# Optimization experiments

Measured on AMD Instinct MI355X. Metric: run time of the kernel, lower is better.

## Reference

```python
import jax, jax.numpy as jnp
import numpy as np

# Mega (Flash-Quad) encoder layer: MultiHeadEMA + moving-average gated chunked attention + ScaleNorm
L, B, D = 2048, 16, 512        # seq_len, batch, embed_dim (fairseq L,B,D layout)
H, Z, NDIM = 1024, 128, 2      # hdim, zdim, EMA ndim
CHUNK = 128                    # Flash-Quad chunk size
MAXPOS = 1024                  # SimpleRelativePositionalBias max positions
EPS = 1e-6                     # ScaleNorm eps


def setup_inputs() -> dict:
    key = jax.random.key(0)
    ks = jax.random.split(key, 16)
    def nrm(k, shape, s=0.02):
        return jax.random.normal(k, shape, jnp.float32) * s
    return dict(
        x=jax.random.normal(ks[0], (L, B, D), jnp.float32),
        # MultiHeadEMA params (bidirectional -> kernel_dim = 2*D)
        ema_delta=nrm(ks[1], (2 * D, NDIM, 1), 1.0),
        ema_alpha=nrm(ks[2], (2 * D, NDIM, 1), 1.0),
        ema_beta=nrm(ks[3], (2 * D, NDIM, 1), 0.02),
        ema_gamma=nrm(ks[4], (2 * D, NDIM), 1.0),
        ema_omega=nrm(ks[5], (D,), 1.0),
        # projections
        Wv=nrm(ks[6], (D, H)), bv=jnp.zeros((H,), jnp.float32),
        Wmx=nrm(ks[7], (D, Z + H + 2 * D)), bmx=jnp.zeros((Z + H + 2 * D,), jnp.float32),
        Wh=nrm(ks[8], (H, D)), bh=jnp.zeros((D,), jnp.float32),
        # per-dim q/k affine (gamma/beta) on shared z
        qk_gamma=nrm(ks[9], (2, Z), 0.1) + 1.0,
        qk_beta=nrm(ks[10], (2, Z), 0.1),
        # simple relative positional bias over chunk length
        rel_pos_bias=nrm(ks[11], (2 * MAXPOS - 1,), 0.02),
        # ScaleNorm scalar
        norm_scalar=jnp.ones((), jnp.float32),
    )


def _ema(x, delta, alpha, beta, gamma, omega):
    """Bidirectional multi-dim damped EMA via FFT convolution. x: (L,B,D) -> (L,B,D)."""
    Lx, Bx, Dx = x.shape
    residual = x * omega
    xt = jnp.transpose(x, (1, 2, 0))                      # B,D,L
    p = jax.nn.sigmoid(delta)                             # 2D,n,1
    q = 1.0 - p * jax.nn.sigmoid(alpha)                   # 2D,n,1 in (0,1)
    vander = jnp.arange(Lx, dtype=jnp.float32)[None, None, :] * jnp.log(q)  # 2D,n,L
    kern = jnp.einsum('dnl,dn->dl', (p * beta) * jnp.exp(vander),
                      gamma * (1.0 / np.sqrt(NDIM)))      # 2D,L
    k1, k2 = kern[:Dx], kern[Dx:]
    # combined causal + anticausal kernel of length 2L-1, input left-padded by L-1
    kc = jnp.pad(k1, ((0, 0), (Lx - 1, 0))) + jnp.pad(k2[:, ::-1], ((0, 0), (0, Lx - 1)))
    xp = jnp.pad(xt, ((0, 0), (0, 0), (Lx - 1, 0)))
    n = 2 * (2 * Lx - 1)
    out = jnp.fft.irfft(jnp.fft.rfft(xp, n=n) * jnp.fft.rfft(kc, n=n), n=n)
    out = out[..., 2 * Lx - 2: 2 * Lx - 2 + Lx]           # B,D,L
    return jax.nn.silu(jnp.transpose(out, (2, 0, 1)) + residual)


def _forward(x, ema_delta, ema_alpha, ema_beta, ema_gamma, ema_omega,
             Wv, bv, Wmx, bmx, Wh, bh, qk_gamma, qk_beta, rel_pos_bias, norm_scalar):
    Lx, Bx, Dx = x.shape
    residual = x
    v = jax.nn.silu(x @ Wv + bv)                          # L,B,H
    mx = _ema(x, ema_delta, ema_alpha, ema_beta, ema_gamma, ema_omega)  # L,B,D
    base = mx @ Wmx + bmx                                 # L,B,D+Z+H+D
    u = jax.nn.sigmoid(base[..., :Dx])                    # update gate
    zr = jax.nn.silu(base[..., Dx:Dx + Z + H])
    hx = base[..., Dx + Z + H:]
    z, r = zr[..., :Z], zr[..., Z:]                       # shared z, reset gate r
    zqk = z[..., None, :] * qk_gamma + qk_beta            # L,B,2,Z
    nc = Lx // CHUNK
    q = jnp.transpose(zqk[..., 0, :], (1, 0, 2)).reshape(Bx, nc, CHUNK, Z)
    k = jnp.transpose(zqk[..., 1, :], (1, 0, 2)).reshape(Bx, nc, CHUNK, Z)
    vc = jnp.transpose(v, (1, 0, 2)).reshape(Bx, nc, CHUNK, H)
    # Toeplitz relative bias: bias[i,j] = rel_pos_bias[MAXPOS-1 + j - i]
    idx = (MAXPOS - 1) + jnp.arange(CHUNK)[None, :] - jnp.arange(CHUNK)[:, None]
    bias = rel_pos_bias[idx]                              # C,C
    qk = jnp.einsum('bnqz,bnkz->bnqk', q * (Z ** -0.5), k) + bias
    attn = jax.nn.softmax(qk, axis=-1)                    # B,nc,C,C
    h = jnp.einsum('bnqk,bnkh->bnqh', attn, vc).reshape(Bx, Lx, H)
    h = jnp.transpose(h, (1, 0, 2))                       # L,B,H
    h = jax.nn.silu(hx + (h * r) @ Wh + bh)               # L,B,D
    out = residual + u * (h - residual)                   # addcmul gated residual
    ms = jnp.mean(out * out, axis=-1, keepdims=True)      # ScaleNorm
    out = norm_scalar * out * jax.lax.rsqrt(ms + EPS)
    return out, attn


def reference(x, ema_delta, ema_alpha, ema_beta, ema_gamma, ema_omega,
              Wv, bv, Wmx, bmx, Wh, bh, qk_gamma, qk_beta, rel_pos_bias, norm_scalar):
    return _forward(x, ema_delta, ema_alpha, ema_beta, ema_gamma, ema_omega,
                    Wv, bv, Wmx, bmx, Wh, bh, qk_gamma, qk_beta, rel_pos_bias, norm_scalar)
```

## Files before the change

### kernel.cpp

```cpp
#include <hip/hip_runtime.h>
#include <math.h>

#define L_DIM 2048
#define B_DIM 16
#define D_DIM 512
#define H_DIM 1024
#define Z_DIM 128
#define NC    16
#define BASE_N 2176
#define ROWS  (L_DIM*B_DIM)
#define NSEG  32
#define SLEN  64
#define CHAINS 8192

typedef unsigned short bf16_t;
typedef __attribute__((ext_vector_type(8))) short short8;
typedef __attribute__((ext_vector_type(4))) float f32x4;

__device__ __forceinline__ float sigmoidf_(float x){ return 1.f/(1.f+__expf(-x)); }
__device__ __forceinline__ float siluf_(float x){ return x/(1.f+__expf(-x)); }
__device__ __forceinline__ float fbits(unsigned int b){ union{unsigned int i; float f;} c; c.i=b; return c.f; }
__device__ __forceinline__ unsigned short f2bf(float f){
  union{float f; unsigned int i;} c; c.f=f;
  unsigned int r = c.i + 0x7FFFu + ((c.i>>16)&1u);
  return (unsigned short)(r>>16);
}
__device__ __forceinline__ float bf2f(unsigned short u){ return fbits(((unsigned int)u)<<16); }

__device__ __forceinline__ void load8(const float* __restrict__ p, float* d){
  float4 a = *(const float4*)p; float4 b = *(const float4*)(p+4);
  d[0]=a.x; d[1]=a.y; d[2]=a.z; d[3]=a.w; d[4]=b.x; d[5]=b.y; d[6]=b.z; d[7]=b.w;
}
__device__ __forceinline__ void load8(const bf16_t* __restrict__ p, float* d){
  uint4 u = *(const uint4*)p;
  d[0]=fbits(u.x<<16); d[1]=fbits(u.x&0xFFFF0000u);
  d[2]=fbits(u.y<<16); d[3]=fbits(u.y&0xFFFF0000u);
  d[4]=fbits(u.z<<16); d[5]=fbits(u.z&0xFFFF0000u);
  d[6]=fbits(u.w<<16); d[7]=fbits(u.w&0xFFFF0000u);
}
__device__ __forceinline__ void store8bf(bf16_t* p, const float* v){
  uint4 s;
  s.x = (unsigned int)f2bf(v[0]) | ((unsigned int)f2bf(v[1])<<16);
  s.y = (unsigned int)f2bf(v[2]) | ((unsigned int)f2bf(v[3])<<16);
  s.z = (unsigned int)f2bf(v[4]) | ((unsigned int)f2bf(v[5])<<16);
  s.w = (unsigned int)f2bf(v[6]) | ((unsigned int)f2bf(v[7])<<16);
  *(uint4*)p = s;
}

__device__ __forceinline__ void glds16(const void* g, void* l) {
  __builtin_amdgcn_global_load_lds(
      (const __attribute__((address_space(1))) unsigned int*)g,
      (__attribute__((address_space(3))) unsigned int*)l, 16, 0, 0);
}

__global__ __launch_bounds__(256) void transpose_cvt_kernel(
    const float* __restrict__ W, bf16_t* __restrict__ Wt, int K, int N)
{
  __shared__ float t[32][33];
  int bx = blockIdx.x, by = blockIdx.y;
  int lx = threadIdx.x & 31, ly = threadIdx.x >> 5;
  #pragma unroll
  for (int i = 0; i < 32; i += 8)
    t[ly+i][lx] = W[(size_t)(by*32+ly+i)*N + bx*32 + lx];
  __syncthreads();
  #pragma unroll
  for (int i = 0; i < 32; i += 8)
    Wt[(size_t)(bx*32+ly+i)*K + by*32 + lx] = f2bf(t[lx][ly+i]);
}

__global__ __launch_bounds__(256) void ema_carry_kernel(
    const float* __restrict__ x, const float* __restrict__ delta,
    const float* __restrict__ alpha, bf16_t* __restrict__ xb,
    float* __restrict__ carry)
{
  int idx = blockIdx.x*256 + threadIdx.x;
  int d = idx & 511, c = idx & 8191, s = idx >> 13;
  float qf0 = 1.f - sigmoidf_(delta[d*2+0])*sigmoidf_(alpha[d*2+0]);
  float qf1 = 1.f - sigmoidf_(delta[d*2+1])*sigmoidf_(alpha[d*2+1]);
  int dd = d + 512;
  float qb0 = 1.f - sigmoidf_(delta[dd*2+0])*sigmoidf_(alpha[dd*2+0]);
  float qb1 = 1.f - sigmoidf_(delta[dd*2+1])*sigmoidf_(alpha[dd*2+1]);
  size_t off = (size_t)s*SLEN*CHAINS + c;
  float h0=0.f, h1=0.f;
  #pragma unroll
  for (int t = 0; t < SLEN; ++t) {
    size_t a = off + (size_t)t*CHAINS;
    float xv = x[a];
    xb[a] = f2bf(xv);
    h0 = fmaf(qf0, h0, xv); h1 = fmaf(qf1, h1, xv);
  }
  float g0=0.f, g1=0.f;
  #pragma unroll
  for (int t = SLEN-1; t >= 0; --t) {
    float xv = bf2f(xb[off + (size_t)t*CHAINS]);
    g0 = fmaf(qb0, g0, xv); g1 = fmaf(qb1, g1, xv);
  }
  carry[(size_t)s*CHAINS + c]              = h0;
  carry[(size_t)s*CHAINS + c + 262144]     = h1;
  carry[(size_t)s*CHAINS + c + 524288]     = g0;
  carry[(size_t)s*CHAINS + c + 786432]     = g1;
}

__global__ __launch_bounds__(256) void ema_combine_kernel(
    const float* __restrict__ delta, const float* __restrict__ alpha,
    float* __restrict__ carry)
{
  int c = blockIdx.x*256 + threadIdx.x;
  int d = c & 511;
  float qf0 = 1.f - sigmoidf_(delta[d*2+0])*sigmoidf_(alpha[d*2+0]);
  float qf1 = 1.f - sigmoidf_(delta[d*2+1])*sigmoidf_(alpha[d*2+1]);
  int dd = d + 512;
  float qb0 = 1.f - sigmoidf_(delta[dd*2+0])*sigmoidf_(alpha[dd*2+0]);
  float qb1 = 1.f - sigmoidf_(delta[dd*2+1])*sigmoidf_(alpha[dd*2+1]);
  float df0=qf0, df1=qf1, db0=qb0, db1=qb1;
  #pragma unroll
  for (int i = 0; i < 6; ++i) { df0*=df0; df1*=df1; db0*=db0; db1*=db1; }
  float h0=0.f, h1=0.f;
  for (int s = 0; s < NSEG; ++s) {
    size_t a = (size_t)s*CHAINS + c;
    float t0 = carry[a], t1 = carry[a+262144];
    carry[a] = h0; carry[a+262144] = h1;
    h0 = fmaf(df0, h0, t0); h1 = fmaf(df1, h1, t1);
  }
  float g0=0.f, g1=0.f;
  for (int s = NSEG-1; s >= 0; --s) {
    size_t a = (size_t)s*CHAINS + c;
    float t0 = carry[a+524288], t1 = carry[a+786432];
    carry[a+524288] = g0; carry[a+786432] = g1;
    g0 = fmaf(db0, g0, t0); g1 = fmaf(db1, g1, t1);
  }
}

__global__ __launch_bounds__(256) void ema_apply_kernel(
    const bf16_t* __restrict__ xb, const float* __restrict__ delta,
    const float* __restrict__ alpha, const float* __restrict__ beta,
    const float* __restrict__ gamma, const float* __restrict__ omega,
    const float* __restrict__ carry, bf16_t* __restrict__ mx)
{
  int idx = blockIdx.x*256 + threadIdx.x;
  int d = idx & 511, c = idx & 8191, s = idx >> 13;
  const float rs = 0.70710678118654752f;
  float pf0 = sigmoidf_(delta[d*2+0]), pf1 = sigmoidf_(delta[d*2+1]);
  float qf0 = 1.f - pf0*sigmoidf_(alpha[d*2+0]);
  float qf1 = 1.f - pf1*sigmoidf_(alpha[d*2+1]);
  float cf0 = pf0*beta[d*2+0]*gamma[d*2+0]*rs;
  float cf1 = pf1*beta[d*2+1]*gamma[d*2+1]*rs;
  int dd = d + 512;
  float pb0 = sigmoidf_(delta[dd*2+0]), pb1 = sigmoidf_(delta[dd*2+1]);
  float qb0 = 1.f - pb0*sigmoidf_(alpha[dd*2+0]);
  float qb1 = 1.f - pb1*sigmoidf_(alpha[dd*2+1]);
  float cb0 = pb0*beta[dd*2+0]*gamma[dd*2+0]*rs;
  float cb1 = pb1*beta[dd*2+1]*gamma[dd*2+1]*rs;
  float om = omega[d];
  size_t off = (size_t)s*SLEN*CHAINS + c;
  float h0 = carry[(size_t)s*CHAINS + c];
  float h1 = carry[(size_t)s*CHAINS + c + 262144];
  float yv[SLEN];
  #pragma unroll
  for (int t = 0; t < SLEN; ++t) {
    float xv = bf2f(xb[off + (size_t)t*CHAINS]);
    h0 = fmaf(qf0, h0, xv); h1 = fmaf(qf1, h1, xv);
    yv[t] = fmaf(cf0, h0, cf1*h1);
  }
  float g0 = carry[(size_t)s*CHAINS + c + 524288];
  float g1 = carry[(size_t)s*CHAINS + c + 786432];
  #pragma unroll
  for (int t = SLEN-1; t >= 0; --t) {
    size_t a = off + (size_t)t*CHAINS;
    float xv = bf2f(xb[a]);
    g0 = fmaf(qb0, g0, xv); g1 = fmaf(qb1, g1, xv);
    float sv = yv[t] + fmaf(cb0, g0, cb1*g1) + xv*om;
    mx[a] = f2bf(siluf_(sv));
  }
}

__global__ __launch_bounds__(256) void mfma_gemm_kernel(
    const bf16_t* __restrict__ A, const bf16_t* __restrict__ Bt,
    const float* __restrict__ bias, const bf16_t* __restrict__ Add, int addLd,
    bf16_t* __restrict__ C, int N, int K, int nT, int act)
{
  __shared__ __align__(16) char smem[34816];
  bf16_t* As = (bf16_t*)smem;
  bf16_t* Bs = (bf16_t*)(smem + 8192);
  bf16_t* Cs = (bf16_t*)smem;
  int flat = blockIdx.x;
  int xcd = flat & 7, g = flat >> 3;
  int mT8 = (int)(gridDim.x / (unsigned)nT) >> 3;
  int mt = xcd*mT8 + g / nT;
  int nt = g % nT;
  int m0 = mt*128, n0 = nt*128;
  int tid = threadIdx.x;
  int wave = tid >> 6, lane = tid & 63;
  int srow = lane >> 2, schunk = lane & 3;
  const bf16_t* Ag0 = A + (size_t)(m0 + wave*16 + srow)*K + schunk*8;
  const bf16_t* Ag1 = Ag0 + (size_t)64*K;
  const bf16_t* Bg0 = Bt + (size_t)(n0 + wave*16 + srow)*K + schunk*8;
  const bf16_t* Bg1 = Bg0 + (size_t)64*K;
  bf16_t* Asl0 = As + (wave*16)*32;
  bf16_t* Asl1 = As + (64 + wave*16)*32;
  bf16_t* Bsl0 = Bs + (wave*16)*32;
  bf16_t* Bsl1 = Bs + (64 + wave*16)*32;

  int wm = wave >> 1, wn = wave & 1;
  int fr = lane & 15, fq = lane >> 4;
  f32x4 acc[4][4];
  #pragma unroll
  for (int i = 0; i < 4; ++i)
    #pragma unroll
    for (int j = 0; j < 4; ++j)
      acc[i][j] = (f32x4){0.f,0.f,0.f,0.f};

  for (int k0 = 0; k0 < K; k0 += 32) {
    __syncthreads();
    glds16(Ag0 + k0, Asl0);
    glds16(Ag1 + k0, Asl1);
    glds16(Bg0 + k0, Bsl0);
    glds16(Bg1 + k0, Bsl1);
    __syncthreads();
    short8 af[4], bfr[4];
    #pragma unroll
    for (int mi = 0; mi < 4; ++mi)
      af[mi] = *(const short8*)&As[(wm*64 + mi*16 + fr)*32 + fq*8];
    #pragma unroll
    for (int ni = 0; ni < 4; ++ni)
      bfr[ni] = *(const short8*)&Bs[(wn*64 + ni*16 + fr)*32 + fq*8];
    #pragma unroll
    for (int mi = 0; mi < 4; ++mi)
      #pragma unroll
      for (int ni = 0; ni < 4; ++ni)
        acc[mi][ni] = __builtin_amdgcn_mfma_f32_16x16x32_bf16(
            af[mi], bfr[ni], acc[mi][ni], 0, 0, 0);
  }

  __syncthreads();
  #pragma unroll
  for (int ni = 0; ni < 4; ++ni) {
    int cl = wn*64 + ni*16 + fr;
    int gn = n0 + cl;
    float bv = bias[gn];
    #pragma unroll
    for (int mi = 0; mi < 4; ++mi) {
      #pragma unroll
      for (int r = 0; r < 4; ++r) {
        int ml = wm*64 + mi*16 + fq*4 + r;
        float val = acc[mi][ni][r] + bv;
        if (Add) val += bf2f(Add[(size_t)(m0+ml)*addLd + gn]);
        if (act == 1) val = siluf_(val);
        Cs[ml*136 + cl] = f2bf(val);
      }
    }
  }
  __syncthreads();
  int row = tid >> 1, c0 = (tid & 1)*64;
  #pragma unroll
  for (int q = 0; q < 8; ++q)
    *(uint4*)(C + (size_t)(m0+row)*N + n0 + c0 + q*8) =
        *(const uint4*)&Cs[row*136 + c0 + q*8];
}

__global__ __launch_bounds__(256) void mfma_gemm_v_kernel(
    const bf16_t* __restrict__ A, const bf16_t* __restrict__ Bt,
    const float* __restrict__ bias, bf16_t* __restrict__ vt, int nT, int K)
{
  __shared__ __align__(16) char smem[34816];
  bf16_t* As = (bf16_t*)smem;
  bf16_t* Bs = (bf16_t*)(smem + 8192);
  bf16_t* Cs = (bf16_t*)smem;
  const int N = H_DIM;
  int flat = blockIdx.x;
  int xcd = flat & 7, g = flat >> 3;
  int mT8 = (int)(gridDim.x / (unsigned)nT) >> 3;
  int mt = xcd*mT8 + g / nT;
  int nt = g % nT;
  int m0 = mt*128, n0 = nt*128;
  int tid = threadIdx.x;
  int wave = tid >> 6, lane = tid & 63;
  int srow = lane >> 2, schunk = lane & 3;
  const bf16_t* Ag0 = A + (size_t)(m0 + wave*16 + srow)*K + schunk*8;
  const bf16_t* Ag1 = Ag0 + (size_t)64*K;
  const bf16_t* Bg0 = Bt + (size_t)(n0 + wave*16 + srow)*K + schunk*8;
  const bf16_t* Bg1 = Bg0 + (size_t)64*K;
  bf16_t* Asl0 = As + (wave*16)*32;
  bf16_t* Asl1 = As + (64 + wave*16)*32;
  bf16_t* Bsl0 = Bs + (wave*16)*32;
  bf16_t* Bsl1 = Bs + (64 + wave*16)*32;

  int wm = wave >> 1, wn = wave & 1;
  int fr = lane & 15, fq = lane >> 4;
  f32x4 acc[4][4];
  #pragma unroll
  for (int i = 0; i < 4; ++i)
    #pragma unroll
    for (int j = 0; j < 4; ++j)
      acc[i][j] = (f32x4){0.f,0.f,0.f,0.f};

  for (int k0 = 0; k0 < K; k0 += 32) {
    __syncthreads();
    glds16(Ag0 + k0, Asl0);
    glds16(Ag1 + k0, Asl1);
    glds16(Bg0 + k0, Bsl0);
    glds16(Bg1 + k0, Bsl1);
    __syncthreads();
    short8 af[4], bfr[4];
    #pragma unroll
    for (int mi = 0; mi < 4; ++mi)
      af[mi] = *(const short8*)&As[(wm*64 + mi*16 + fr)*32 + fq*8];
    #pragma unroll
    for (int ni = 0; ni < 4; ++ni)
      bfr[ni] = *(const short8*)&Bs[(wn*64 + ni*16 + fr)*32 + fq*8];
    #pragma unroll
    for (int mi = 0; mi < 4; ++mi)
      #pragma unroll
      for (int ni = 0; ni < 4; ++ni)
        acc[mi][ni] = __builtin_amdgcn_mfma_f32_16x16x32_bf16(
            af[mi], bfr[ni], acc[mi][ni], 0, 0, 0);
  }

  __syncthreads();
  #pragma unroll
  for (int ni = 0; ni < 4; ++ni) {
    int cl = wn*64 + ni*16 + fr;
    float bv = bias[n0 + cl];
    #pragma unroll
    for (int mi = 0; mi < 4; ++mi) {
      #pragma unroll
      for (int r = 0; r < 4; ++r) {
        int ml = wm*64 + mi*16 + fq*4 + r;
        Cs[ml*136 + cl] = f2bf(siluf_(acc[mi][ni][r] + bv));
      }
    }
  }
  __syncthreads();
  int b = tid >> 4, h0l = (tid & 15)*8;
  int nchunk = mt >> 4, kbase = (mt & 15)*8;
  #pragma unroll
  for (int j = 0; j < 8; ++j) {
    int hl = h0l + j;
    uint4 s;
    unsigned int w0 = (unsigned int)Cs[(0*16 + b)*136 + hl] |
                      ((unsigned int)Cs[(1*16 + b)*136 + hl] << 16);
    unsigned int w1 = (unsigned int)Cs[(2*16 + b)*136 + hl] |
                      ((unsigned int)Cs[(3*16 + b)*136 + hl] << 16);
    unsigned int w2 = (unsigned int)Cs[(4*16 + b)*136 + hl] |
                      ((unsigned int)Cs[(5*16 + b)*136 + hl] << 16);
    unsigned int w3 = (unsigned int)Cs[(6*16 + b)*136 + hl] |
                      ((unsigned int)Cs[(7*16 + b)*136 + hl] << 16);
    s.x=w0; s.y=w1; s.z=w2; s.w=w3;
    *(uint4*)&vt[((size_t)(b*NC + nchunk)*H_DIM + n0 + hl)*128 + kbase] = s;
  }
}

__global__ __launch_bounds__(256) void attn_scores_mfma_kernel(
    const bf16_t* __restrict__ base, const float* __restrict__ qkg,
    const float* __restrict__ qkb, const float* __restrict__ rpb,
    float* __restrict__ attn_out, bf16_t* __restrict__ p_bf)
{
  __shared__ bf16_t qs[128*136];
  __shared__ bf16_t ks[128*136];
  int blk = blockIdx.x;
  int b = blk >> 4, n = blk & 15;
  int tid = threadIdx.x;
  {
    int r = tid >> 1, z0 = (tid & 1)*64;
    size_t rowoff = ((size_t)((n*128 + r)*B_DIM + b))*BASE_N + 512 + z0;
    #pragma unroll
    for (int cchunk = 0; cchunk < 8; ++cchunk) {
      float t8[8], qv[8], kv[8];
      load8(base + rowoff + cchunk*8, t8);
      #pragma unroll
      for (int j = 0; j < 8; ++j) {
        int z = z0 + cchunk*8 + j;
        float zs = siluf_(t8[j]);
        qv[j] = fmaf(zs, qkg[z],     qkb[z]);
        kv[j] = fmaf(zs, qkg[128+z], qkb[128+z]);
      }
      store8bf(&qs[r*136 + z0 + cchunk*8], qv);
      store8bf(&ks[r*136 + z0 + cchunk*8], kv);
    }
  }
  __syncthreads();
  int wave = tid >> 6, lane = tid & 63;
  int fr = lane & 15, fq = lane >> 4;
  f32x4 acc[2][8];
  #pragma unroll
  for (int i = 0; i < 2; ++i)
    #pragma unroll
    for (int j = 0; j < 8; ++j)
      acc[i][j] = (f32x4){0.f,0.f,0.f,0.f};
  #pragma unroll
  for (int kk = 0; kk < 4; ++kk) {
    short8 af[2], bfr[8];
    #pragma unroll
    for (int mi = 0; mi < 2; ++mi)
      af[mi] = *(const short8*)&qs[(wave*32 + mi*16 + fr)*136 + kk*32 + fq*8];
    #pragma unroll
    for (int ni = 0; ni < 8; ++ni)
      bfr[ni] = *(const short8*)&ks[(ni*16 + fr)*136 + kk*32 + fq*8];
    #pragma unroll
    for (int mi = 0; mi < 2; ++mi)
      #pragma unroll
      for (int ni = 0; ni < 8; ++ni)
        acc[mi][ni] = __builtin_amdgcn_mfma_f32_16x16x32_bf16(
            af[mi], bfr[ni], acc[mi][ni], 0, 0, 0);
  }
  const float scale = 0.08838834764831845f;
  float mrow[2][4], srow[2][4];
  #pragma unroll
  for (int mi = 0; mi < 2; ++mi)
    #pragma unroll
    for (int r = 0; r < 4; ++r) mrow[mi][r] = -1e30f;
  #pragma unroll
  for (int mi = 0; mi < 2; ++mi)
    #pragma unroll
    for (int ni = 0; ni < 8; ++ni)
      #pragma unroll
      for (int r = 0; r < 4; ++r) {
        int i = wave*32 + mi*16 + fq*4 + r;
        int j = ni*16 + fr;
        float v = fmaf(acc[mi][ni][r], scale, rpb[1023 + j - i]);
        acc[mi][ni][r] = v;
        mrow[mi][r] = fmaxf(mrow[mi][r], v);
      }
  #pragma unroll
  for (int mi = 0; mi < 2; ++mi)
    #pragma unroll
    for (int r = 0; r < 4; ++r) {
      float m = mrow[mi][r];
      m = fmaxf(m, __shfl_xor(m, 1));
      m = fmaxf(m, __shfl_xor(m, 2));
      m = fmaxf(m, __shfl_xor(m, 4));
      m = fmaxf(m, __shfl_xor(m, 8));
      mrow[mi][r] = m;
      srow[mi][r] = 0.f;
    }
  #pragma unroll
  for (int mi = 0; mi < 2; ++mi)
    #pragma unroll
    for (int ni = 0; ni < 8; ++ni)
      #pragma unroll
      for (int r = 0; r < 4; ++r) {
        float e = __expf(acc[mi][ni][r] - mrow[mi][r]);
        acc[mi][ni][r] = e;
        srow[mi][r] += e;
      }
  #pragma unroll
  for (int mi = 0; mi < 2; ++mi)
    #pragma unroll
    for (int r = 0; r < 4; ++r) {
      float s = srow[mi][r];
      s += __shfl_xor(s, 1);
      s += __shfl_xor(s, 2);
      s += __shfl_xor(s, 4);
      s += __shfl_xor(s, 8);
      srow[mi][r] = 1.f/s;
    }
  #pragma unroll
  for (int mi = 0; mi < 2; ++mi)
    #pragma unroll
    for (int r = 0; r < 4; ++r) {
      int i = wave*32 + mi*16 + fq*4 + r;
      size_t o = ((size_t)blk*128 + i)*128;
      #pragma unroll
      for (int ni = 0; ni < 8; ++ni) {
        float val = acc[mi][ni][r]*srow[mi][r];
        attn_out[o + ni*16 + fr] = val;
        p_bf[o + ni*16 + fr] = f2bf(val);
      }
    }
}

__global__ __launch_bounds__(256) void attn_pv_kernel(
    const bf16_t* __restrict__ p_bf, const bf16_t* __restrict__ vt,
    const bf16_t* __restrict__ base, bf16_t* __restrict__ hr)
{
  __shared__ __align__(16) char smem[34816];
  bf16_t* As = (bf16_t*)smem;
  bf16_t* Bs = (bf16_t*)(smem + 8192);
  bf16_t* Cs = (bf16_t*)smem;
  int blk = blockIdx.x >> 3, ht = blockIdx.x & 7;
  int b = blk >> 4, n = blk & 15;
  const int K = 128;
  int tid = threadIdx.x;
  int wave = tid >> 6, lane = tid & 63;
  int srow = lane >> 2, schunk = lane & 3;
  const bf16_t* A = p_bf + (size_t)blk*(128*128);
  const bf16_t* Bt = vt + ((size_t)blk*H_DIM + ht*128)*128;
  const bf16_t* Ag0 = A + (size_t)(wave*16 + srow)*K + schunk*8;
  const bf16_t* Ag1 = Ag0 + (size_t)64*K;
  const bf16_t* Bg0 = Bt + (size_t)(wave*16 + srow)*K + schunk*8;
  const bf16_t* Bg1 = Bg0 + (size_t)64*K;
  bf16_t* Asl0 = As + (wave*16)*32;
  bf16_t* Asl1 = As + (64 + wave*16)*32;
  bf16_t* Bsl0 = Bs + (wave*16)*32;
  bf16_t* Bsl1 = Bs + (64 + wave*16)*32;

  int wm = wave >> 1, wn = wave & 1;
  int fr = lane & 15, fq = lane >> 4;
  f32x4 acc[4][4];
  #pragma unroll
  for (int i = 0; i < 4; ++i)
    #pragma unroll
    for (int j = 0; j < 4; ++j)
      acc[i][j] = (f32x4){0.f,0.f,0.f,0.f};

  for (int k0 = 0; k0 < K; k0 += 32) {
    __syncthreads();
    glds16(Ag0 + k0, Asl0);
    glds16(Ag1 + k0, Asl1);
    glds16(Bg0 + k0, Bsl0);
    glds16(Bg1 + k0, Bsl1);
    __syncthreads();
    short8 af[4], bfr[4];
    #pragma unroll
    for (int mi = 0; mi < 4; ++mi)
      af[mi] = *(const short8*)&As[(wm*64 + mi*16 + fr)*32 + fq*8];
    #pragma unroll
    for (int ni = 0; ni < 4; ++ni)
      bfr[ni] = *(const short8*)&Bs[(wn*64 + ni*16 + fr)*32 + fq*8];
    #pragma unroll
    for (int mi = 0; mi < 4; ++mi)
      #pragma unroll
      for (int ni = 0; ni < 4; ++ni)
        acc[mi][ni] = __builtin_amdgcn_mfma_f32_16x16x32_bf16(
            af[mi], bfr[ni], acc[mi][ni], 0, 0, 0);
  }

  __syncthreads();
  #pragma unroll
  for (int ni = 0; ni < 4; ++ni) {
    int cl = wn*64 + ni*16 + fr;
    int hg = ht*128 + cl;
    #pragma unroll
    for (int mi = 0; mi < 4; ++mi) {
      #pragma unroll
      for (int r = 0; r < 4; ++r) {
        int ml = wm*64 + mi*16 + fq*4 + r;
        size_t rowg = (size_t)((n*128 + ml)*B_DIM + b);
        float rg = bf2f(base[rowg*BASE_N + 640 + hg]);
        Cs[ml*136 + cl] = f2bf(acc[mi][ni][r]*siluf_(rg));
      }
    }
  }
  __syncthreads();
  int row = tid >> 1, c0 = (tid & 1)*64;
  size_t rowg = (size_t)((n*128 + row)*B_DIM + b);
  #pragma unroll
  for (int q = 0; q < 8; ++q)
    *(uint4*)(hr + rowg*H_DIM + ht*128 + c0 + q*8) =
        *(const uint4*)&Cs[row*136 + c0 + q*8];
}

__global__ __launch_bounds__(64) void final_kernel(
    const float* __restrict__ x, const bf16_t* __restrict__ h2,
    const bf16_t* __restrict__ base, const float* __restrict__ ns,
    float* __restrict__ out)
{
  int row = blockIdx.x;
  int t = threadIdx.x;
  size_t ro = (size_t)row*D_DIM + t*8;
  float xv[8]; load8(x + ro, xv);
  float hv[8]; load8(h2 + ro, hv);
  float uv[8]; load8(base + (size_t)row*BASE_N + t*8, uv);
  float o[8];
  float ss = 0.f;
  #pragma unroll
  for (int i = 0; i < 8; ++i) {
    float u = sigmoidf_(uv[i]);
    o[i] = xv[i] + u*(hv[i] - xv[i]);
    ss += o[i]*o[i];
  }
  #pragma unroll
  for (int m = 1; m < 64; m <<= 1) ss += __shfl_xor(ss, m);
  float inv = rsqrtf(ss*(1.f/(float)D_DIM) + 1e-6f) * ns[0];
  float4 r0, r1;
  r0.x = o[0]*inv; r0.y = o[1]*inv; r0.z = o[2]*inv; r0.w = o[3]*inv;
  r1.x = o[4]*inv; r1.y = o[5]*inv; r1.z = o[6]*inv; r1.w = o[7]*inv;
  *(float4*)(out + ro) = r0;
  *(float4*)(out + ro + 4) = r1;
}

extern "C" void kernel_launch(void* const* d_in, const int* in_sizes, int n_in,
                              void* d_out, int out_size, void* d_ws, size_t ws_size,
                              hipStream_t stream)
{
  const float* x     = (const float*)d_in[0];
  const float* delta = (const float*)d_in[1];
  const float* alpha = (const float*)d_in[2];
  const float* beta  = (const float*)d_in[3];
  const float* gamma = (const float*)d_in[4];
  const float* omega = (const float*)d_in[5];
  const float* Wv    = (const float*)d_in[6];
  const float* bv    = (const float*)d_in[7];
  const float* Wmx   = (const float*)d_in[8];
  const float* bmx   = (const float*)d_in[9];
  const float* Wh    = (const float*)d_in[10];
  const float* bh    = (const float*)d_in[11];
  const float* qkg   = (const float*)d_in[12];
  const float* qkb   = (const float*)d_in[13];
  const float* rpb   = (const float*)d_in[14];
  const float* ns    = (const float*)d_in[15];

  float* out  = (float*)d_out;
  float* attn = out + (size_t)ROWS*D_DIM;

  char* outb = (char*)d_out;
  bf16_t* x_bf  = (bf16_t*)outb;
  bf16_t* p_bf  = (bf16_t*)outb;
  bf16_t* Wv_t  = (bf16_t*)(outb + 33554432ull);
  bf16_t* Wmx_t = (bf16_t*)(outb + 34603008ull);
  bf16_t* Wh_t  = (bf16_t*)(outb + 36831232ull);

  const size_t WS_NEED = 310378496ull;
  if (ws_size < WS_NEED) return;
  char* wsb = (char*)d_ws;
  bf16_t* mx_bf   = (bf16_t*)(wsb);
  bf16_t* vt      = (bf16_t*)(wsb + 33554432ull);
  bf16_t* base_bf = (bf16_t*)(wsb + 100663296ull);
  bf16_t* hr_bf   = (bf16_t*)(wsb + 243269632ull);
  float*  carry   = (float*)(wsb + 100663296ull);
  bf16_t* h2_bf   = mx_bf;

  transpose_cvt_kernel<<<dim3(32, 16), 256, 0, stream>>>(Wv,  Wv_t,  512, 1024);
  transpose_cvt_kernel<<<dim3(68, 16), 256, 0, stream>>>(Wmx, Wmx_t, 512, 2176);
  transpose_cvt_kernel<<<dim3(16, 32), 256, 0, stream>>>(Wh,  Wh_t,  1024, 512);
  ema_carry_kernel<<<1024, 256, 0, stream>>>(x, delta, alpha, x_bf, carry);
  ema_combine_kernel<<<32, 256, 0, stream>>>(delta, alpha, carry);
  ema_apply_kernel<<<1024, 256, 0, stream>>>(x_bf, delta, alpha, beta, gamma,
                                             omega, carry, mx_bf);
  mfma_gemm_v_kernel<<<2048, 256, 0, stream>>>(x_bf, Wv_t, bv, vt, 8, D_DIM);
  mfma_gemm_kernel<<<4352, 256, 0, stream>>>(
      mx_bf, Wmx_t, bmx, nullptr, 0, base_bf, BASE_N, D_DIM, 17, 0);
  attn_scores_mfma_kernel<<<B_DIM*NC, 256, 0, stream>>>(
      base_bf, qkg, qkb, rpb, attn, p_bf);
  attn_pv_kernel<<<2048, 256, 0, stream>>>(p_bf, vt, base_bf, hr_bf);
  mfma_gemm_kernel<<<1024, 256, 0, stream>>>(
      hr_bf, Wh_t, bh, base_bf + 1664, BASE_N, h2_bf, D_DIM, H_DIM, 4, 1);
  final_kernel<<<ROWS, 64, 0, stream>>>(x, h2_bf, base_bf, ns, out);
}
```

Baseline: 678.5 us.

## Double GEMM K-step to 64 with XOR-swizzled LDS and merge weight transposes

The shared MFMA GEMM main loop now stages 64-wide K slices per iteration instead of 32, which halves the number of barrier pairs per tile. The LDS layout is rotated per row so fragment reads avoid bank conflicts. The three weight transpose/convert launches are merged into one launch to cut launch overhead. The cost is a larger LDS footprint for the staged tiles, and the loop still has no double buffering.

```diff
diff --git a/kernel.cpp b/kernel.cpp
--- a/kernel.cpp
+++ b/kernel.cpp
@@ -53,11 +53,17 @@
       (__attribute__((address_space(3))) unsigned int*)l, 16, 0, 0);
 }
 
-__global__ __launch_bounds__(256) void transpose_cvt_kernel(
-    const float* __restrict__ W, bf16_t* __restrict__ Wt, int K, int N)
+__global__ __launch_bounds__(256) void transpose_all_kernel(
+    const float* __restrict__ Wv, const float* __restrict__ Wmx,
+    const float* __restrict__ Wh, bf16_t* __restrict__ Wvt,
+    bf16_t* __restrict__ Wmxt, bf16_t* __restrict__ Wht)
 {
   __shared__ float t[32][33];
-  int bx = blockIdx.x, by = blockIdx.y;
+  int blk = blockIdx.x;
+  const float* W; bf16_t* Wt; int K, N, bx, by;
+  if (blk < 512)       { W=Wv;  Wt=Wvt;  K=512;  N=1024; bx=blk&31;  by=blk>>5; }
+  else if (blk < 1600) { blk-=512;  W=Wmx; Wt=Wmxt; K=512;  N=2176; bx=blk%68; by=blk/68; }
+  else                 { blk-=1600; W=Wh;  Wt=Wht;  K=1024; N=512;  bx=blk&15; by=blk>>4; }
   int lx = threadIdx.x & 31, ly = threadIdx.x >> 5;
   #pragma unroll
   for (int i = 0; i < 32; i += 8)
@@ -174,6 +180,44 @@
   }
 }
 
+#define GEMM_PROLOG(Aptr, Bptr, Kdim)                                        \
+  int tid = threadIdx.x;                                                     \
+  int wave = tid >> 6, lane = tid & 63;                                      \
+  int lrow = lane >> 3, lchunk = ((lane & 7) - lrow) & 7;                    \
+  const bf16_t* Ag = (Aptr) + (size_t)(wave*32 + lrow)*(Kdim) + lchunk*8;    \
+  const bf16_t* Bg = (Bptr) + (size_t)(wave*32 + lrow)*(Kdim) + lchunk*8;    \
+  int wm = wave >> 1, wn = wave & 1;                                         \
+  int fr = lane & 15, fq = lane >> 4;                                        \
+  f32x4 acc[4][4];                                                           \
+  _Pragma("unroll") for (int i = 0; i < 4; ++i)                              \
+    _Pragma("unroll") for (int j = 0; j < 4; ++j)                            \
+      acc[i][j] = (f32x4){0.f,0.f,0.f,0.f};
+
+#define GEMM_KLOOP(Kdim)                                                     \
+  for (int k0 = 0; k0 < (Kdim); k0 += 64) {                                  \
+    __syncthreads();                                                         \
+    _Pragma("unroll") for (int j = 0; j < 4; ++j) {                          \
+      glds16(Ag + (size_t)j*8*(Kdim) + k0, As + (wave*32 + j*8)*64);         \
+      glds16(Bg + (size_t)j*8*(Kdim) + k0, Bs + (wave*32 + j*8)*64);         \
+    }                                                                        \
+    __syncthreads();                                                         \
+    _Pragma("unroll") for (int kk = 0; kk < 2; ++kk) {                       \
+      short8 af[4], bfr[4];                                                  \
+      _Pragma("unroll") for (int mi = 0; mi < 4; ++mi) {                     \
+        int R = wm*64 + mi*16 + fr;                                          \
+        af[mi] = *(const short8*)&As[R*64 + (((kk<<2)+fq+R)&7)*8];           \
+      }                                                                      \
+      _Pragma("unroll") for (int ni = 0; ni < 4; ++ni) {                     \
+        int R = wn*64 + ni*16 + fr;                                          \
+        bfr[ni] = *(const short8*)&Bs[R*64 + (((kk<<2)+fq+R)&7)*8];          \
+      }                                                                      \
+      _Pragma("unroll") for (int mi = 0; mi < 4; ++mi)                       \
+        _Pragma("unroll") for (int ni = 0; ni < 4; ++ni)                     \
+          acc[mi][ni] = __builtin_amdgcn_mfma_f32_16x16x32_bf16(             \
+              af[mi], bfr[ni], acc[mi][ni], 0, 0, 0);                        \
+    }                                                                        \
+  }
+
 __global__ __launch_bounds__(256) void mfma_gemm_kernel(
     const bf16_t* __restrict__ A, const bf16_t* __restrict__ Bt,
     const float* __restrict__ bias, const bf16_t* __restrict__ Add, int addLd,
@@ -181,7 +225,7 @@
 {
   __shared__ __align__(16) char smem[34816];
   bf16_t* As = (bf16_t*)smem;
-  bf16_t* Bs = (bf16_t*)(smem + 8192);
+  bf16_t* Bs = (bf16_t*)(smem + 16384);
   bf16_t* Cs = (bf16_t*)smem;
   int flat = blockIdx.x;
   int xcd = flat & 7, g = flat >> 3;
@@ -189,49 +233,8 @@
   int mt = xcd*mT8 + g / nT;
   int nt = g % nT;
   int m0 = mt*128, n0 = nt*128;
-  int tid = threadIdx.x;
-  int wave = tid >> 6, lane = tid & 63;
-  int srow = lane >> 2, schunk = lane & 3;
-  const bf16_t* Ag0 = A + (size_t)(m0 + wave*16 + srow)*K + schunk*8;
-  const bf16_t* Ag1 = Ag0 + (size_t)64*K;
-  const bf16_t* Bg0 = Bt + (size_t)(n0 + wave*16 + srow)*K + schunk*8;
-  const bf16_t* Bg1 = Bg0 + (size_t)64*K;
-  bf16_t* Asl0 = As + (wave*16)*32;
-  bf16_t* Asl1 = As + (64 + wave*16)*32;
-  bf16_t* Bsl0 = Bs + (wave*16)*32;
-  bf16_t* Bsl1 = Bs + (64 + wave*16)*32;
-
-  int wm = wave >> 1, wn = wave & 1;
-  int fr = lane & 15, fq = lane >> 4;
-  f32x4 acc[4][4];
-  #pragma unroll
-  for (int i = 0; i < 4; ++i)
-    #pragma unroll
-    for (int j = 0; j < 4; ++j)
-      acc[i][j] = (f32x4){0.f,0.f,0.f,0.f};
-
-  for (int k0 = 0; k0 < K; k0 += 32) {
-    __syncthreads();
-    glds16(Ag0 + k0, Asl0);
-    glds16(Ag1 + k0, Asl1);
-    glds16(Bg0 + k0, Bsl0);
-    glds16(Bg1 + k0, Bsl1);
-    __syncthreads();
-    short8 af[4], bfr[4];
-    #pragma unroll
-    for (int mi = 0; mi < 4; ++mi)
-      af[mi] = *(const short8*)&As[(wm*64 + mi*16 + fr)*32 + fq*8];
-    #pragma unroll
-    for (int ni = 0; ni < 4; ++ni)
-      bfr[ni] = *(const short8*)&Bs[(wn*64 + ni*16 + fr)*32 + fq*8];
-    #pragma unroll
-    for (int mi = 0; mi < 4; ++mi)
-      #pragma unroll
-      for (int ni = 0; ni < 4; ++ni)
-        acc[mi][ni] = __builtin_amdgcn_mfma_f32_16x16x32_bf16(
-            af[mi], bfr[ni], acc[mi][ni], 0, 0, 0);
-  }
-
+  GEMM_PROLOG(A + (size_t)m0*K, Bt + (size_t)n0*K, K)
+  GEMM_KLOOP(K)
   __syncthreads();
   #pragma unroll
   for (int ni = 0; ni < 4; ++ni) {
@@ -264,58 +267,16 @@
 {
   __shared__ __align__(16) char smem[34816];
   bf16_t* As = (bf16_t*)smem;
-  bf16_t* Bs = (bf16_t*)(smem + 8192);
+  bf16_t* Bs = (bf16_t*)(smem + 16384);
   bf16_t* Cs = (bf16_t*)smem;
-  const int N = H_DIM;
   int flat = blockIdx.x;
   int xcd = flat & 7, g = flat >> 3;
   int mT8 = (int)(gridDim.x / (unsigned)nT) >> 3;
   int mt = xcd*mT8 + g / nT;
   int nt = g % nT;
   int m0 = mt*128, n0 = nt*128;
-  int tid = threadIdx.x;
-  int wave = tid >> 6, lane = tid & 63;
-  int srow = lane >> 2, schunk = lane & 3;
-  const bf16_t* Ag0 = A + (size_t)(m0 + wave*16 + srow)*K + schunk*8;
-  const bf16_t* Ag1 = Ag0 + (size_t)64*K;
-  const bf16_t* Bg0 = Bt + (size_t)(n0 + wave*16 + srow)*K + schunk*8;
-  const bf16_t* Bg1 = Bg0 + (size_t)64*K;
-  bf16_t* Asl0 = As + (wave*16)*32;
-  bf16_t* Asl1 = As + (64 + wave*16)*32;
-  bf16_t* Bsl0 = Bs + (wave*16)*32;
-  bf16_t* Bsl1 = Bs + (64 + wave*16)*32;
-
-  int wm = wave >> 1, wn = wave & 1;
-  int fr = lane & 15, fq = lane >> 4;
-  f32x4 acc[4][4];
-  #pragma unroll
-  for (int i = 0; i < 4; ++i)
-    #pragma unroll
-    for (int j = 0; j < 4; ++j)
-      acc[i][j] = (f32x4){0.f,0.f,0.f,0.f};
-
-  for (int k0 = 0; k0 < K; k0 += 32) {
-    __syncthreads();
-    glds16(Ag0 + k0, Asl0);
-    glds16(Ag1 + k0, Asl1);
-    glds16(Bg0 + k0, Bsl0);
-    glds16(Bg1 + k0, Bsl1);
-    __syncthreads();
-    short8 af[4], bfr[4];
-    #pragma unroll
-    for (int mi = 0; mi < 4; ++mi)
-      af[mi] = *(const short8*)&As[(wm*64 + mi*16 + fr)*32 + fq*8];
-    #pragma unroll
-    for (int ni = 0; ni < 4; ++ni)
-      bfr[ni] = *(const short8*)&Bs[(wn*64 + ni*16 + fr)*32 + fq*8];
-    #pragma unroll
-    for (int mi = 0; mi < 4; ++mi)
-      #pragma unroll
-      for (int ni = 0; ni < 4; ++ni)
-        acc[mi][ni] = __builtin_amdgcn_mfma_f32_16x16x32_bf16(
-            af[mi], bfr[ni], acc[mi][ni], 0, 0, 0);
-  }
-
+  GEMM_PROLOG(A + (size_t)m0*K, Bt + (size_t)n0*K, K)
+  GEMM_KLOOP(K)
   __syncthreads();
   #pragma unroll
   for (int ni = 0; ni < 4; ++ni) {
@@ -337,15 +298,14 @@
   for (int j = 0; j < 8; ++j) {
     int hl = h0l + j;
     uint4 s;
-    unsigned int w0 = (unsigned int)Cs[(0*16 + b)*136 + hl] |
-                      ((unsigned int)Cs[(1*16 + b)*136 + hl] << 16);
-    unsigned int w1 = (unsigned int)Cs[(2*16 + b)*136 + hl] |
-                      ((unsigned int)Cs[(3*16 + b)*136 + hl] << 16);
-    unsigned int w2 = (unsigned int)Cs[(4*16 + b)*136 + hl] |
-                      ((unsigned int)Cs[(5*16 + b)*136 + hl] << 16);
-    unsigned int w3 = (unsigned int)Cs[(6*16 + b)*136 + hl] |
-                      ((unsigned int)Cs[(7*16 + b)*136 + hl] << 16);
-    s.x=w0; s.y=w1; s.z=w2; s.w=w3;
+    s.x = (unsigned int)Cs[(0*16 + b)*136 + hl] |
+          ((unsigned int)Cs[(1*16 + b)*136 + hl] << 16);
+    s.y = (unsigned int)Cs[(2*16 + b)*136 + hl] |
+          ((unsigned int)Cs[(3*16 + b)*136 + hl] << 16);
+    s.z = (unsigned int)Cs[(4*16 + b)*136 + hl] |
+          ((unsigned int)Cs[(5*16 + b)*136 + hl] << 16);
+    s.w = (unsigned int)Cs[(6*16 + b)*136 + hl] |
+          ((unsigned int)Cs[(7*16 + b)*136 + hl] << 16);
     *(uint4*)&vt[((size_t)(b*NC + nchunk)*H_DIM + n0 + hl)*128 + kbase] = s;
   }
 }
@@ -475,56 +435,14 @@
 {
   __shared__ __align__(16) char smem[34816];
   bf16_t* As = (bf16_t*)smem;
-  bf16_t* Bs = (bf16_t*)(smem + 8192);
+  bf16_t* Bs = (bf16_t*)(smem + 16384);
   bf16_t* Cs = (bf16_t*)smem;
   int blk = blockIdx.x >> 3, ht = blockIdx.x & 7;
   int b = blk >> 4, n = blk & 15;
   const int K = 128;
-  int tid = threadIdx.x;
-  int wave = tid >> 6, lane = tid & 63;
-  int srow = lane >> 2, schunk = lane & 3;
-  const bf16_t* A = p_bf + (size_t)blk*(128*128);
-  const bf16_t* Bt = vt + ((size_t)blk*H_DIM + ht*128)*128;
-  const bf16_t* Ag0 = A + (size_t)(wave*16 + srow)*K + schunk*8;
-  const bf16_t* Ag1 = Ag0 + (size_t)64*K;
-  const bf16_t* Bg0 = Bt + (size_t)(wave*16 + srow)*K + schunk*8;
-  const bf16_t* Bg1 = Bg0 + (size_t)64*K;
-  bf16_t* Asl0 = As + (wave*16)*32;
-  bf16_t* Asl1 = As + (64 + wave*16)*32;
-  bf16_t* Bsl0 = Bs + (wave*16)*32;
-  bf16_t* Bsl1 = Bs + (64 + wave*16)*32;
-
-  int wm = wave >> 1, wn = wave & 1;
-  int fr = lane & 15, fq = lane >> 4;
-  f32x4 acc[4][4];
-  #pragma unroll
-  for (int i = 0; i < 4; ++i)
-    #pragma unroll
-    for (int j = 0; j < 4; ++j)
-      acc[i][j] = (f32x4){0.f,0.f,0.f,0.f};
-
-  for (int k0 = 0; k0 < K; k0 += 32) {
-    __syncthreads();
-    glds16(Ag0 + k0, Asl0);
-    glds16(Ag1 + k0, Asl1);
-    glds16(Bg0 + k0, Bsl0);
-    glds16(Bg1 + k0, Bsl1);
-    __syncthreads();
-    short8 af[4], bfr[4];
-    #pragma unroll
-    for (int mi = 0; mi < 4; ++mi)
-      af[mi] = *(const short8*)&As[(wm*64 + mi*16 + fr)*32 + fq*8];
-    #pragma unroll
-    for (int ni = 0; ni < 4; ++ni)
-      bfr[ni] = *(const short8*)&Bs[(wn*64 + ni*16 + fr)*32 + fq*8];
-    #pragma unroll
-    for (int mi = 0; mi < 4; ++mi)
-      #pragma unroll
-      for (int ni = 0; ni < 4; ++ni)
-        acc[mi][ni] = __builtin_amdgcn_mfma_f32_16x16x32_bf16(
-            af[mi], bfr[ni], acc[mi][ni], 0, 0, 0);
-  }
-
+  GEMM_PROLOG(p_bf + (size_t)blk*(128*128),
+              vt + ((size_t)blk*H_DIM + ht*128)*128, K)
+  GEMM_KLOOP(K)
   __syncthreads();
   #pragma unroll
   for (int ni = 0; ni < 4; ++ni) {
@@ -620,9 +538,7 @@
   float*  carry   = (float*)(wsb + 100663296ull);
   bf16_t* h2_bf   = mx_bf;
 
-  transpose_cvt_kernel<<<dim3(32, 16), 256, 0, stream>>>(Wv,  Wv_t,  512, 1024);
-  transpose_cvt_kernel<<<dim3(68, 16), 256, 0, stream>>>(Wmx, Wmx_t, 512, 2176);
-  transpose_cvt_kernel<<<dim3(16, 32), 256, 0, stream>>>(Wh,  Wh_t,  1024, 512);
+  transpose_all_kernel<<<2112, 256, 0, stream>>>(Wv, Wmx, Wh, Wv_t, Wmx_t, Wh_t);
   ema_carry_kernel<<<1024, 256, 0, stream>>>(x, delta, alpha, x_bf, carry);
   ema_combine_kernel<<<32, 256, 0, stream>>>(delta, alpha, carry);
   ema_apply_kernel<<<1024, 256, 0, stream>>>(x_bf, delta, alpha, beta, gamma,
```

New measurement: 650.0 us. 4.2% less time.
